# Performance work log

Measured on AMD Instinct MI355X. Metric: run time of the kernel, lower is better.

Reference implementation:

```python
import jax, jax.numpy as jnp
import numpy as np

INPUT, HIDDEN, OUTPUT = 512, 1024, 512

def setup_inputs() -> dict:
    key = jax.random.key(0)
    ks = jax.random.split(key, 7)
    s_in = 1.0 / np.sqrt(INPUT)
    s_h = 1.0 / np.sqrt(HIDDEN)
    return {
        "x": jax.random.normal(ks[0], (64, 512, INPUT), dtype=jnp.float32),
        "W_in": jax.random.uniform(ks[1], (INPUT, HIDDEN), minval=-s_in, maxval=s_in, dtype=jnp.float32),
        "b_in": jax.random.uniform(ks[2], (HIDDEN,), minval=-s_in, maxval=s_in, dtype=jnp.float32),
        "W_h": jax.random.uniform(ks[3], (HIDDEN, HIDDEN), minval=-s_h, maxval=s_h, dtype=jnp.float32),
        "b_h": jax.random.uniform(ks[4], (HIDDEN,), minval=-s_h, maxval=s_h, dtype=jnp.float32),
        "W_out": jax.random.uniform(ks[5], (HIDDEN, OUTPUT), minval=-s_h, maxval=s_h, dtype=jnp.float32),
        "b_out": jax.random.uniform(ks[6], (OUTPUT,), minval=-s_h, maxval=s_h, dtype=jnp.float32),
    }

def reference(x, W_in, b_in, W_h, b_h, W_out, b_out):
    B = x.shape[0]
    # Precompute input projection for all timesteps: [B, T, H]
    xin = jnp.einsum('bti,ih->bth', x, W_in) + b_in
    h0 = jnp.zeros((B, W_h.shape[0]), dtype=x.dtype)

    def step(h, xin_t):
        h_new = jnp.tanh(xin_t + h @ W_h + b_h)
        return h_new, None

    h_final, _ = jax.lax.scan(step, h0, jnp.swapaxes(xin, 0, 1))  # scan over T
    return h_final @ W_out + b_out
```

## Files before the change

### kernel.cpp

```cpp
#include <hip/hip_runtime.h>


typedef float f32x4 __attribute__((ext_vector_type(4)));
typedef short bf16x8 __attribute__((ext_vector_type(8)));
typedef short s16x4 __attribute__((ext_vector_type(4)));
typedef unsigned u32;
typedef unsigned u32x2 __attribute__((ext_vector_type(2)));
typedef unsigned u32x4 __attribute__((ext_vector_type(4)));

__device__ __forceinline__ short f2bf(float f) {
  unsigned u = __builtin_bit_cast(unsigned, f);
  u = (u + 0x7FFFu + ((u >> 16) & 1u)) >> 16;
  return (short)u;
}
__device__ __forceinline__ float bf2f(short s) {
  unsigned u = ((unsigned)(unsigned short)s) << 16;
  return __builtin_bit_cast(float, u);
}

__global__ __launch_bounds__(256) void k_prep(const float* __restrict__ Wh,
                                              short* __restrict__ wprep) {
  const int wgid = blockIdx.x;
  const int cj = wgid >> 2, wslot = wgid & 3;
  const int tid = threadIdx.x, lane = tid & 63, sub = tid >> 6;
  const int l15 = lane & 15, lhi = lane >> 4;
  #pragma unroll
  for (int ktl = 0; ktl < 2; ++ktl) {
    int kt = sub * 2 + ktl;
    #pragma unroll
    for (int nt = 0; nt < 4; ++nt) {
      const float* src = Wh + (size_t)(wslot * 256 + kt * 32 + lhi * 8) * 1024
                            + cj * 64 + nt * 16 + l15;
      bf16x8 v;
      #pragma unroll
      for (int j = 0; j < 8; ++j) v[j] = f2bf(src[(size_t)j * 1024]);
      *(bf16x8*)(wprep + ((((size_t)(cj * 4 + wslot) * 8 + kt) * 4 + nt) * 64 + lane) * 8) = v;
    }
  }
}

__global__ __launch_bounds__(256) void k_inproj(const float* __restrict__ X,
                                                const float* __restrict__ Win,
                                                const float* __restrict__ bin,
                                                short* __restrict__ xin) {
  __shared__ __align__(16) short Al[128][40];
  __shared__ __align__(16) short Bl[128][40];
  __shared__ __align__(16) short Cl[128][64];
  const int m0g = blockIdx.x * 128, n0g = blockIdx.y * 128;
  const int tid = threadIdx.x;
  const int lane = tid & 63, wave = tid >> 6;
  const int wm = (wave & 1) * 64, wn = (wave >> 1) * 64;
  const int l15 = lane & 15, lhi = lane >> 4;

  f32x4 acc[4][4] = {};

  for (int kb = 0; kb < 512; kb += 32) {
    #pragma unroll
    for (int i = 0; i < 4; ++i) {
      int flat = tid + i * 256;
      int row = flat >> 3, k4 = (flat & 7) * 4;
      float4 v = *(const float4*)(X + (size_t)(m0g + row) * 512 + kb + k4);
      s16x4 s; s[0] = f2bf(v.x); s[1] = f2bf(v.y); s[2] = f2bf(v.z); s[3] = f2bf(v.w);
      *(s16x4*)&Al[row][k4] = s;
    }
    #pragma unroll
    for (int i = 0; i < 4; ++i) {
      int flat = tid + i * 256;
      int n = flat & 127, k0 = (flat >> 7) * 4;
      const float* wp = Win + (size_t)(kb + k0) * 1024 + n0g + n;
      s16x4 s;
      s[0] = f2bf(wp[0]); s[1] = f2bf(wp[1024]); s[2] = f2bf(wp[2048]); s[3] = f2bf(wp[3072]);
      *(s16x4*)&Bl[n][k0] = s;
    }
    __syncthreads();
    bf16x8 a[4], b[4];
    #pragma unroll
    for (int mt = 0; mt < 4; ++mt) a[mt] = *(const bf16x8*)&Al[wm + mt * 16 + l15][lhi * 8];
    #pragma unroll
    for (int nt = 0; nt < 4; ++nt) b[nt] = *(const bf16x8*)&Bl[wn + nt * 16 + l15][lhi * 8];
    #pragma unroll
    for (int mt = 0; mt < 4; ++mt)
      #pragma unroll
      for (int nt = 0; nt < 4; ++nt)
        acc[mt][nt] = __builtin_amdgcn_mfma_f32_16x16x32_bf16(a[mt], b[nt], acc[mt][nt], 0, 0, 0);
    __syncthreads();
  }

  float bias[4];
  #pragma unroll
  for (int nt = 0; nt < 4; ++nt) bias[nt] = bin[n0g + wn + nt * 16 + l15];

  const size_t gbase = ((size_t)(m0g >> 13) * 512 + (m0g & 511)) * 16 + ((m0g >> 9) & 15);
  #pragma unroll
  for (int h = 0; h < 2; ++h) {
    if ((wave >> 1) == h) {
      #pragma unroll
      for (int mt = 0; mt < 4; ++mt)
        #pragma unroll
        for (int nt = 0; nt < 4; ++nt)
          #pragma unroll
          for (int r = 0; r < 4; ++r) {
            int row = wm + mt * 16 + lhi * 4 + r;
            Cl[row][nt * 16 + l15] = f2bf(acc[mt][nt][r] + bias[nt]);
          }
    }
    __syncthreads();
    {
      int row = tid >> 1, c0 = (tid & 1) * 32;
      const int4* src = (const int4*)&Cl[row][c0];
      int4* dst = (int4*)(xin + (gbase + (size_t)row * 16) * 1024 + n0g + h * 64 + c0);
      dst[0] = src[0]; dst[1] = src[1]; dst[2] = src[2]; dst[3] = src[3];
    }
    __syncthreads();
  }
}

__global__ __launch_bounds__(256, 1) void k_recur(const short* __restrict__ xin,
                                                  const short* __restrict__ wprep,
                                                  const float* __restrict__ bh,
                                                  short* __restrict__ hfrag,
                                                  u32* __restrict__ flags,
                                                  float* __restrict__ hfin) {
  const int wg = blockIdx.x;
  const int g = wg & 3, cj = wg >> 2;
  const int tid = threadIdx.x, lane = tid & 63, wave = tid >> 6;
  const int l15 = lane & 15, lhi = lane >> 4;
  const int colbase = cj << 6, rowbase = g << 4;
  __shared__ __align__(16) float part[4][16][68];

  bf16x8 wf[8][4];
  {
    const short* wb = wprep + ((size_t)(cj * 4 + wave) << 14) + lane * 8;
    #pragma unroll
    for (int kt = 0; kt < 8; ++kt)
      #pragma unroll
      for (int nt = 0; nt < 4; ++nt) {
        u32x4 r;
        const short* ap = wb + ((kt * 4 + nt) << 9);
        asm volatile("global_load_dwordx4 %0, %1, off" : "=v"(r) : "v"(ap) : "memory");
        wf[kt][nt] = __builtin_bit_cast(bf16x8, r);
      }
    asm volatile("s_waitcnt vmcnt(0)" ::: "memory");
    __builtin_amdgcn_sched_barrier(0);
  }

  const int erow = tid >> 4, ec0 = (tid & 15) << 2;
  const int n0 = colbase + ec0;
  const float4 bh4 = *(const float4*)(bh + n0);
  const short* xbase = xin + (size_t)g * 512 * 16384 + erow * 1024 + n0;
  const u32* fp = flags + (g << 10) + (cj << 6) + (wave << 4) + (lane & 3);
  u32* myflag = flags + (g << 10) + (tid << 6) + ((cj >> 2) << 4) + (cj & 3);
  const short* hrd0 = hfrag + ((g << 2) + wave) * 4096 + lane * 8;
  const short* hrd1 = hrd0 + 2048;
  const int wk = n0 >> 8, ktp = (n0 >> 5) & 7, e = n0 & 31;
  const int plane = ((e >> 3) << 4) | erow, pj = n0 & 7;
  short* hwr = hfrag + (((((g << 2) + wk) << 3) + ktp) << 9) + (plane << 3) + pj;

  {
    s16x4 xs = *(const s16x4*)xbase;
    float h0 = tanhf(bh4.x + bf2f(xs[0]));
    float h1 = tanhf(bh4.y + bf2f(xs[1]));
    float h2 = tanhf(bh4.z + bf2f(xs[2]));
    float h3 = tanhf(bh4.w + bf2f(xs[3]));
    u32x2 wv;
    wv[0] = ((u32)(unsigned short)f2bf(h1) << 16) | (unsigned short)f2bf(h0);
    wv[1] = ((u32)(unsigned short)f2bf(h3) << 16) | (unsigned short)f2bf(h2);
    short* dst = hwr + 65536;
    asm volatile("global_store_dwordx2 %0, %1, off sc1" :: "v"(dst), "v"(wv) : "memory");
    asm volatile("s_waitcnt vmcnt(0)" ::: "memory");
    __syncthreads();
    if (tid < 16) {
      u32 fv = 1;
      asm volatile("global_store_dword %0, %1, off sc1" :: "v"(myflag), "v"(fv) : "memory");
    }
  }

  for (int t = 1; t < 512; ++t) {
    s16x4 xs = *(const s16x4*)(xbase + (size_t)t * 16384);
    for (;;) {
      u32 f;
      asm volatile("global_load_dword %0, %1, off sc1\n\ts_waitcnt vmcnt(0)"
                   : "=v"(f) : "v"(fp) : "memory");
      __builtin_amdgcn_sched_barrier(0);
      if (__all((int)(f >= (u32)t))) break;
    }
    const int poff = (t & 1) << 16;
    const short* hs0 = hrd0 + poff;
    const short* hs1 = hrd1 + poff;
    u32x4 ar[8];
    #pragma unroll
    for (int kt = 0; kt < 4; ++kt) {
      asm volatile("global_load_dwordx4 %0, %1, off offset:%c2 sc1"
                   : "=v"(ar[kt]) : "v"(hs0), "i"(kt * 1024) : "memory");
      asm volatile("global_load_dwordx4 %0, %1, off offset:%c2 sc1"
                   : "=v"(ar[kt + 4]) : "v"(hs1), "i"(kt * 1024) : "memory");
    }
    asm volatile("s_waitcnt vmcnt(0)" ::: "memory");
    __builtin_amdgcn_sched_barrier(0);

    f32x4 acc[4] = {};
    #pragma unroll
    for (int kt = 0; kt < 8; ++kt) {
      bf16x8 a = __builtin_bit_cast(bf16x8, ar[kt]);
      #pragma unroll
      for (int nt = 0; nt < 4; ++nt)
        acc[nt] = __builtin_amdgcn_mfma_f32_16x16x32_bf16(a, wf[kt][nt], acc[nt], 0, 0, 0);
    }
    #pragma unroll
    for (int nt = 0; nt < 4; ++nt)
      #pragma unroll
      for (int rr = 0; rr < 4; ++rr)
        part[wave][lhi * 4 + rr][nt * 16 + l15] = acc[nt][rr];
    __syncthreads();

    f32x4 p0 = *(const f32x4*)&part[0][erow][ec0];
    f32x4 p1 = *(const f32x4*)&part[1][erow][ec0];
    f32x4 p2 = *(const f32x4*)&part[2][erow][ec0];
    f32x4 p3 = *(const f32x4*)&part[3][erow][ec0];
    f32x4 ps = (p0 + p1) + (p2 + p3);
    float h0 = tanhf(ps[0] + bh4.x + bf2f(xs[0]));
    float h1 = tanhf(ps[1] + bh4.y + bf2f(xs[1]));
    float h2 = tanhf(ps[2] + bh4.z + bf2f(xs[2]));
    float h3 = tanhf(ps[3] + bh4.w + bf2f(xs[3]));

    if (t < 511) {
      u32x2 wv;
      wv[0] = ((u32)(unsigned short)f2bf(h1) << 16) | (unsigned short)f2bf(h0);
      wv[1] = ((u32)(unsigned short)f2bf(h3) << 16) | (unsigned short)f2bf(h2);
      short* dst = hwr + (((t + 1) & 1) << 16);
      asm volatile("global_store_dwordx2 %0, %1, off sc1" :: "v"(dst), "v"(wv) : "memory");
      asm volatile("s_waitcnt vmcnt(0)" ::: "memory");
      __syncthreads();
      if (tid < 16) {
        u32 fv = (u32)(t + 1);
        asm volatile("global_store_dword %0, %1, off sc1" :: "v"(myflag), "v"(fv) : "memory");
      }
    } else {
      float4 hf4; hf4.x = h0; hf4.y = h1; hf4.z = h2; hf4.w = h3;
      *(float4*)(hfin + (rowbase + erow) * 1024 + n0) = hf4;
      __syncthreads();
    }
  }
}

__global__ __launch_bounds__(256) void k_out(const float* __restrict__ hfin,
                                             const float* __restrict__ Wout,
                                             const float* __restrict__ bout,
                                             float* __restrict__ out) {
  __shared__ __align__(16) float hrow[1024];
  const int b = blockIdx.x >> 1;
  const int c0 = (blockIdx.x & 1) << 8;
  const int tid = threadIdx.x;
  #pragma unroll
  for (int i = 0; i < 4; ++i) hrow[tid + i * 256] = hfin[b * 1024 + tid + i * 256];
  __syncthreads();
  const int col = c0 + tid;
  const float* wp = Wout + col;
  float a0 = bout[col], a1 = 0, a2 = 0, a3 = 0, a4 = 0, a5 = 0, a6 = 0, a7 = 0;
  #pragma unroll 4
  for (int k = 0; k < 1024; k += 8) {
    a0 += hrow[k + 0] * wp[(size_t)(k + 0) * 512];
    a1 += hrow[k + 1] * wp[(size_t)(k + 1) * 512];
    a2 += hrow[k + 2] * wp[(size_t)(k + 2) * 512];
    a3 += hrow[k + 3] * wp[(size_t)(k + 3) * 512];
    a4 += hrow[k + 4] * wp[(size_t)(k + 4) * 512];
    a5 += hrow[k + 5] * wp[(size_t)(k + 5) * 512];
    a6 += hrow[k + 6] * wp[(size_t)(k + 6) * 512];
    a7 += hrow[k + 7] * wp[(size_t)(k + 7) * 512];
  }
  out[b * 512 + col] = ((a0 + a1) + (a2 + a3)) + ((a4 + a5) + (a6 + a7));
}

extern "C" void kernel_launch(void* const* d_in, const int* in_sizes, int n_in,
                              void* d_out, int out_size, void* d_ws, size_t ws_size,
                              hipStream_t stream) {
  const float* x    = (const float*)d_in[0];
  const float* Win  = (const float*)d_in[1];
  const float* bin  = (const float*)d_in[2];
  const float* Wh   = (const float*)d_in[3];
  const float* bh   = (const float*)d_in[4];
  const float* Wout = (const float*)d_in[5];
  const float* bout = (const float*)d_in[6];

  char* ws = (char*)d_ws;
  short* xin   = (short*)ws;
  short* wprep = (short*)(ws + 67108864);
  short* hfrag = (short*)(ws + 69206016);
  u32*   flags = (u32*)(ws + 69468160);
  float* hfin  = (float*)(ws + 69484544);

  hipMemsetAsync(flags, 0, 16384, stream);
  hipLaunchKernelGGL(k_prep, dim3(64), dim3(256), 0, stream, Wh, wprep);
  hipLaunchKernelGGL(k_inproj, dim3(256, 8), dim3(256), 0, stream, x, Win, bin, xin);
  hipLaunchKernelGGL(k_recur, dim3(64), dim3(256), 0, stream,
                     xin, wprep, bh, hfrag, flags, hfin);
  hipLaunchKernelGGL(k_out, dim3(128), dim3(256), 0, stream, hfin, Wout, bout, (float*)d_out);
}
```

Before: 1.296 ms.

## Use per-wave flags, triple-buffer hidden state, and double-buffer LDS partials

Each wave now publishes its own readiness flag once its store lands, replacing the block-wide barrier before flag publication, and readers poll 16 flags per wave instead of 4. The hidden-state exchange buffer goes from two slots to three, and the LDS partial-sum buffer is double-buffered. Together these remove one workgroup barrier per timestep and the write-after-read hazard that barrier guarded. The cost is more flag reads per poll and a larger workspace, which shifts the flags and hfin offsets.

```diff
diff --git a/kernel.cpp b/kernel.cpp
--- a/kernel.cpp
+++ b/kernel.cpp
@@ -126,7 +126,7 @@
   const int tid = threadIdx.x, lane = tid & 63, wave = tid >> 6;
   const int l15 = lane & 15, lhi = lane >> 4;
   const int colbase = cj << 6, rowbase = g << 4;
-  __shared__ __align__(16) float part[4][16][68];
+  __shared__ __align__(16) float part[2][4][16][68];
 
   bf16x8 wf[8][4];
   {
@@ -148,8 +148,9 @@
   const int n0 = colbase + ec0;
   const float4 bh4 = *(const float4*)(bh + n0);
   const short* xbase = xin + (size_t)g * 512 * 16384 + erow * 1024 + n0;
-  const u32* fp = flags + (g << 10) + (cj << 6) + (wave << 4) + (lane & 3);
-  u32* myflag = flags + (g << 10) + (tid << 6) + ((cj >> 2) << 4) + (cj & 3);
+  const u32* fp = flags + (g << 10) + (cj << 6) + (wave << 4) + (lane & 15);
+  u32* myflag = flags + (g << 10) + (lane << 6) + ((cj >> 2) << 4)
+                      + ((cj & 3) << 2) + wave;
   const short* hrd0 = hfrag + ((g << 2) + wave) * 4096 + lane * 8;
   const short* hrd1 = hrd0 + 2048;
   const int wk = n0 >> 8, ktp = (n0 >> 5) & 7, e = n0 & 31;
@@ -168,13 +169,14 @@
     short* dst = hwr + 65536;
     asm volatile("global_store_dwordx2 %0, %1, off sc1" :: "v"(dst), "v"(wv) : "memory");
     asm volatile("s_waitcnt vmcnt(0)" ::: "memory");
-    __syncthreads();
-    if (tid < 16) {
+    __builtin_amdgcn_sched_barrier(0);
+    if (lane < 16) {
       u32 fv = 1;
       asm volatile("global_store_dword %0, %1, off sc1" :: "v"(myflag), "v"(fv) : "memory");
     }
   }
 
+  int rd = 1;
   for (int t = 1; t < 512; ++t) {
     s16x4 xs = *(const s16x4*)(xbase + (size_t)t * 16384);
     for (;;) {
@@ -184,7 +186,7 @@
       __builtin_amdgcn_sched_barrier(0);
       if (__all((int)(f >= (u32)t))) break;
     }
-    const int poff = (t & 1) << 16;
+    const int poff = rd << 16;
     const short* hs0 = hrd0 + poff;
     const short* hs1 = hrd1 + poff;
     u32x4 ar[8];
@@ -206,39 +208,41 @@
       for (int nt = 0; nt < 4; ++nt)
         acc[nt] = __builtin_amdgcn_mfma_f32_16x16x32_bf16(a, wf[kt][nt], acc[nt], 0, 0, 0);
     }
+    const int p = t & 1;
     #pragma unroll
     for (int nt = 0; nt < 4; ++nt)
       #pragma unroll
       for (int rr = 0; rr < 4; ++rr)
-        part[wave][lhi * 4 + rr][nt * 16 + l15] = acc[nt][rr];
-    __syncthreads();
-
-    f32x4 p0 = *(const f32x4*)&part[0][erow][ec0];
-    f32x4 p1 = *(const f32x4*)&part[1][erow][ec0];
-    f32x4 p2 = *(const f32x4*)&part[2][erow][ec0];
-    f32x4 p3 = *(const f32x4*)&part[3][erow][ec0];
+        part[p][wave][lhi * 4 + rr][nt * 16 + l15] = acc[nt][rr];
+    __syncthreads();
+
+    f32x4 p0 = *(const f32x4*)&part[p][0][erow][ec0];
+    f32x4 p1 = *(const f32x4*)&part[p][1][erow][ec0];
+    f32x4 p2 = *(const f32x4*)&part[p][2][erow][ec0];
+    f32x4 p3 = *(const f32x4*)&part[p][3][erow][ec0];
     f32x4 ps = (p0 + p1) + (p2 + p3);
     float h0 = tanhf(ps[0] + bh4.x + bf2f(xs[0]));
     float h1 = tanhf(ps[1] + bh4.y + bf2f(xs[1]));
     float h2 = tanhf(ps[2] + bh4.z + bf2f(xs[2]));
     float h3 = tanhf(ps[3] + bh4.w + bf2f(xs[3]));
 
+    rd = (rd == 2) ? 0 : rd + 1;
+
     if (t < 511) {
       u32x2 wv;
       wv[0] = ((u32)(unsigned short)f2bf(h1) << 16) | (unsigned short)f2bf(h0);
       wv[1] = ((u32)(unsigned short)f2bf(h3) << 16) | (unsigned short)f2bf(h2);
-      short* dst = hwr + (((t + 1) & 1) << 16);
+      short* dst = hwr + (rd << 16);
       asm volatile("global_store_dwordx2 %0, %1, off sc1" :: "v"(dst), "v"(wv) : "memory");
       asm volatile("s_waitcnt vmcnt(0)" ::: "memory");
-      __syncthreads();
-      if (tid < 16) {
+      __builtin_amdgcn_sched_barrier(0);
+      if (lane < 16) {
         u32 fv = (u32)(t + 1);
         asm volatile("global_store_dword %0, %1, off sc1" :: "v"(myflag), "v"(fv) : "memory");
       }
     } else {
       float4 hf4; hf4.x = h0; hf4.y = h1; hf4.z = h2; hf4.w = h3;
       *(float4*)(hfin + (rowbase + erow) * 1024 + n0) = hf4;
-      __syncthreads();
     }
   }
 }
@@ -286,8 +290,8 @@
   short* xin   = (short*)ws;
   short* wprep = (short*)(ws + 67108864);
   short* hfrag = (short*)(ws + 69206016);
-  u32*   flags = (u32*)(ws + 69468160);
-  float* hfin  = (float*)(ws + 69484544);
+  u32*   flags = (u32*)(ws + 69599232);
+  float* hfin  = (float*)(ws + 69615616);
 
   hipMemsetAsync(flags, 0, 16384, stream);
   hipLaunchKernelGGL(k_prep, dim3(64), dim3(256), 0, stream, Wh, wprep);
```

Result: slower. 1.727 ms (+33.3%).
